# Performance work log

Hardware: AMD Instinct MI355X
Metric: run time of the kernel (lower is better)

Reference implementation:

```python
import jax, jax.numpy as jnp
import numpy as np

N_NODES = 10000
N_EDGES = 160000
F_IN, D, N_CLS = 300, 1024, 10
NEG_SLOPE = 0.2


def setup_inputs() -> dict:
    key = jax.random.key(0)
    ks = jax.random.split(key, 12)
    s = 0.05  # small init scale for numerical sanity
    return {
        "x": jax.random.normal(ks[0], (N_NODES, F_IN), jnp.float32),
        "edge_index": jax.random.randint(ks[1], (2, N_EDGES), 0, N_NODES, jnp.int64),
        "W1": jax.random.normal(ks[2], (F_IN, D), jnp.float32) * s,
        "att_src1": jax.random.normal(ks[3], (D,), jnp.float32) * s,
        "att_dst1": jax.random.normal(ks[4], (D,), jnp.float32) * s,
        "b1": jnp.zeros((D,), jnp.float32),
        "W2": jax.random.normal(ks[5], (D, D), jnp.float32) * s,
        "att_src2": jax.random.normal(ks[6], (D,), jnp.float32) * s,
        "att_dst2": jax.random.normal(ks[7], (D,), jnp.float32) * s,
        "b2": jnp.zeros((D,), jnp.float32),
        "fc_w": jax.random.normal(ks[8], (D, N_CLS), jnp.float32) * s,
        "fc_b": jnp.zeros((N_CLS,), jnp.float32),
    }


def gat_conv(x, src, dst, W, a_src, a_dst, b):
    # PyG GATConv, heads=1: h = x W; e_ij = leaky_relu(a_src.h_j + a_dst.h_i)
    h = x @ W                      # [N, D]
    e = jax.nn.leaky_relu((h @ a_src)[src] + (h @ a_dst)[dst], NEG_SLOPE)  # [E]
    # scatter-softmax over edges grouped by destination node
    m = jax.lax.stop_gradient(jax.ops.segment_max(e, dst, num_segments=N_NODES))
    ex = jnp.exp(e - m[dst])
    denom = jax.ops.segment_sum(ex, dst, num_segments=N_NODES)
    alpha = ex / denom[dst]        # [E]
    out = jax.ops.segment_sum(alpha[:, None] * h[src], dst, num_segments=N_NODES)
    return out + b


def reference(x, edge_index, W1, att_src1, att_dst1, b1,
              W2, att_src2, att_dst2, b2, fc_w, fc_b):
    loops = jnp.arange(N_NODES, dtype=edge_index.dtype)
    src = jnp.concatenate([edge_index[0], loops])  # add_self_loops=True
    dst = jnp.concatenate([edge_index[1], loops])
    emb = jax.nn.relu(gat_conv(x, src, dst, W1, att_src1, att_dst1, b1))
    emb = jax.nn.relu(gat_conv(emb, src, dst, W2, att_src2, att_dst2, b2))
    return jax.nn.softmax(emb @ fc_w + fc_b, axis=-1)
```

## Files before the change

### kernel.cpp

```cpp
#include <hip/hip_runtime.h>
#include <hip/hip_bf16.h>
#include <hip/hip_fp16.h>
#include <math.h>

#define N_NODES 10000
#define N_EDGES 160000
#define E_TOT   (N_EDGES + N_NODES)
#define F_IN    300
#define D       1024
#define N_CLS   10
#define NEG_SLOPE 0.2f

#define MP      10112
#define KP1     320
#define KP2     1024
#define WCAP    1024

typedef __attribute__((ext_vector_type(8))) _Float16 f16x8;
typedef __attribute__((ext_vector_type(4))) float f32x4;

#define GLOAD_LDS16(g, l) __builtin_amdgcn_global_load_lds( \
    (const __attribute__((address_space(1))) void*)(g), \
    (__attribute__((address_space(3))) void*)(l), 16, 0, 0)


__global__ void count_edges(const int* __restrict__ dst, int* __restrict__ deg) {
    int e = blockIdx.x * blockDim.x + threadIdx.x;
    if (e < N_EDGES) atomicAdd(&deg[dst[e]], 1);
}

__global__ void scan_offs(const int* __restrict__ deg, int* __restrict__ offs,
                          int* __restrict__ pos) {
    __shared__ int sbuf[1024];
    __shared__ int scarry;
    int t = threadIdx.x;
    if (t == 0) { scarry = 0; offs[0] = 0; }
    __syncthreads();
    for (int base = 0; base < N_NODES; base += 1024) {
        int v = (base + t < N_NODES) ? deg[base + t] : 0;
        sbuf[t] = v;
        __syncthreads();
        for (int off = 1; off < 1024; off <<= 1) {
            int add = (t >= off) ? sbuf[t - off] : 0;
            __syncthreads();
            sbuf[t] += add;
            __syncthreads();
        }
        int carry = scarry;
        if (base + t < N_NODES) {
            int incl = carry + sbuf[t];
            offs[base + t + 1] = incl;
            pos[base + t]      = incl - v;
        }
        __syncthreads();
        if (t == 1023) scarry = carry + sbuf[1023];
        __syncthreads();
    }
}

__global__ void scatter_edges(const int* __restrict__ src, const int* __restrict__ dst,
                              int* __restrict__ pos, int* __restrict__ ssrc) {
    int e = blockIdx.x * blockDim.x + threadIdx.x;
    if (e < N_EDGES) {
        int d = dst[e];
        int p = atomicAdd(&pos[d], 1);
        ssrc[p] = src[e];
    } else if (e < E_TOT) {
        int i = e - N_EDGES;
        int p = atomicAdd(&pos[i], 1);
        ssrc[p] = i;
    }
}


#define ZR1 (112 * KP1)
#define ZR2 (N_NODES * 20)
#define ZR3 (112 * KP2)
#define ZTOT (2*ZR1 + 2*ZR2 + 2*ZR3 + 2*N_NODES)

#define ZONE_A 331
#define ZONE_B 320
#define ZONE_C 1024
#define ZONE_D ((ZTOT + N_NODES + 255) / 256)

__global__ __launch_bounds__(256) void mega_prep(
        const float* __restrict__ W1, const float* __restrict__ as1,
        const float* __restrict__ ad1, const float* __restrict__ W2,
        const float* __restrict__ as2, const float* __restrict__ ad2,
        float* __restrict__ u1, float* __restrict__ v1,
        float* __restrict__ u2, float* __restrict__ v2,
        _Float16* __restrict__ BT1h, _Float16* __restrict__ BT2h,
        float* __restrict__ hs2, float* __restrict__ hd2,
        unsigned short* __restrict__ Ah1, unsigned short* __restrict__ Al1,
        unsigned short* __restrict__ Ah2, unsigned short* __restrict__ Al2,
        int* __restrict__ deg) {
    __shared__ float tile[32][33];
    int b = blockIdx.x;
    int t = threadIdx.x;

    if (b < ZONE_A) {
        int wid  = (b * 256 + t) >> 6;
        int lane = t & 63;
        const float* row; const float* a; const float* bb; float *du, *dv; int k;
        if (wid < F_IN) {
            k = wid; row = W1 + (size_t)k * D; a = as1; bb = ad1; du = u1; dv = v1;
        } else {
            k = wid - F_IN; row = W2 + (size_t)k * D; a = as2; bb = ad2; du = u2; dv = v2;
        }
        float s1 = 0.f, s2 = 0.f;
        for (int n = lane; n < D; n += 64) {
            float w = row[n];
            s1 += w * a[n];
            s2 += w * bb[n];
        }
        #pragma unroll
        for (int o = 32; o; o >>= 1) { s1 += __shfl_xor(s1, o); s2 += __shfl_xor(s2, o); }
        if (lane == 0) { du[k] = s1; dv[k] = s2; }
        return;
    }
    if (b < ZONE_A + ZONE_B + ZONE_C) {
        if (b < ZONE_A + ZONE_B) {
            int b2 = b - ZONE_A;
            int kb = b2 % (KP1 / 32), nb = b2 / (KP1 / 32);
            int k0 = kb * 32, n0 = nb * 32;
            int tx = t & 31, ty = t >> 5;
            #pragma unroll
            for (int j = 0; j < 32; j += 8) {
                int k = k0 + ty + j;
                tile[ty + j][tx] = (k < F_IN) ? W1[(size_t)k * D + n0 + tx] : 0.f;
            }
            __syncthreads();
            #pragma unroll
            for (int j = 0; j < 32; j += 8)
                BT1h[(size_t)(n0 + ty + j) * KP1 + k0 + tx] = (_Float16)tile[tx][ty + j];
        } else {
            int b2 = b - ZONE_A - ZONE_B;
            int kb = b2 & 31, nb = b2 >> 5;
            int k0 = kb * 32, n0 = nb * 32;
            int tx = t & 31, ty = t >> 5;
            #pragma unroll
            for (int j = 0; j < 32; j += 8) {
                int k = k0 + ty + j;
                tile[ty + j][tx] = W2[(size_t)k * D + n0 + tx];
            }
            __syncthreads();
            #pragma unroll
            for (int j = 0; j < 32; j += 8)
                BT2h[(size_t)(n0 + ty + j) * KP2 + k0 + tx] = (_Float16)tile[tx][ty + j];
        }
        return;
    }
    int idx = (b - ZONE_A - ZONE_B - ZONE_C) * 256 + t;
    if (idx >= ZTOT + N_NODES) return;
    if (idx >= ZTOT) { deg[idx - ZTOT] = 1; return; }
    if (idx < 2 * ZR1) {
        unsigned short* B = (idx < ZR1) ? Ah1 : Al1;
        int off = (idx < ZR1) ? idx : idx - ZR1;
        B[(size_t)N_NODES * KP1 + off] = 0;
    } else if ((idx -= 2 * ZR1) < 2 * ZR2) {
        unsigned short* B = (idx < ZR2) ? Ah1 : Al1;
        int off = (idx < ZR2) ? idx : idx - ZR2;
        int r = off / 20, c = 300 + off % 20;
        B[(size_t)r * KP1 + c] = 0;
    } else if ((idx -= 2 * ZR2) < 2 * ZR3) {
        unsigned short* B = (idx < ZR3) ? Ah2 : Al2;
        int off = (idx < ZR3) ? idx : idx - ZR3;
        B[(size_t)N_NODES * KP2 + off] = 0;
    } else {
        idx -= 2 * ZR3;
        if (idx < N_NODES) hs2[idx] = 0.f;
        else hd2[idx - N_NODES] = 0.f;
    }
}


__global__ void node_scores_x(const float* __restrict__ x, const float* __restrict__ u1,
                              const float* __restrict__ v1, float* __restrict__ hs,
                              float* __restrict__ hd) {
    int wid  = (int)((blockIdx.x * blockDim.x + threadIdx.x) >> 6);
    int lane = threadIdx.x & 63;
    if (wid >= N_NODES) return;
    const float* row = x + (size_t)wid * F_IN;
    float s1 = 0.f, s2 = 0.f;
    for (int k = lane; k < F_IN; k += 64) {
        float v = row[k];
        s1 += v * u1[k];
        s2 += v * v1[k];
    }
    #pragma unroll
    for (int o = 32; o; o >>= 1) { s1 += __shfl_xor(s1, o); s2 += __shfl_xor(s2, o); }
    if (lane == 0) { hs[wid] = s1; hd[wid] = s2; }
}


__global__ __launch_bounds__(256) void aggregate_x(
        const float* __restrict__ x, const float* __restrict__ hs,
        const float* __restrict__ hd, const int* __restrict__ offs,
        const int* __restrict__ ssrc, _Float16* __restrict__ outh,
        _Float16* __restrict__ outl) {
    int i = blockIdx.x;
    int t = threadIdx.x;
    int lane = t & 63;
    int wv = t >> 6;
    int start = offs[i], end = offs[i + 1];
    __shared__ float red[8];
    __shared__ float part[2][75][5];
    __shared__ float wcache[WCAP];
    float hdi = hd[i];

    float lmax = -INFINITY;
    for (int p = start + t; p < end; p += 256) {
        float s = hs[ssrc[p]] + hdi;
        s = (s >= 0.f) ? s : s * NEG_SLOPE;
        lmax = fmaxf(lmax, s);
    }
    #pragma unroll
    for (int o = 32; o; o >>= 1) lmax = fmaxf(lmax, __shfl_xor(lmax, o));
    if (lane == 0) red[wv] = lmax;
    __syncthreads();
    float m = fmaxf(fmaxf(red[0], red[1]), fmaxf(red[2], red[3]));

    float lsum = 0.f;
    for (int p = start + t; p < end; p += 256) {
        float s = hs[ssrc[p]] + hdi;
        s = (s >= 0.f) ? s : s * NEG_SLOPE;
        float ex = __expf(s - m);
        int q = p - start;
        if (q < WCAP) wcache[q] = ex;
        lsum += ex;
    }
    #pragma unroll
    for (int o = 32; o; o >>= 1) lsum += __shfl_xor(lsum, o);
    if (lane == 0) red[4 + wv] = lsum;
    __syncthreads();
    float inv = 1.0f / (red[4] + red[5] + red[6] + red[7]);
    bool cached = (end - start) <= WCAP;

    int g = t / 75;
    int s = t - g * 75;
    int c = s * 4;
    float4 a = {0.f, 0.f, 0.f, 0.f};
    if (t < 225) {
        int p = start + g;
        for (; p + 3 < end; p += 6) {
            int j0 = ssrc[p], j1 = ssrc[p + 3];
            float w0, w1;
            if (cached) { w0 = wcache[p - start]; w1 = wcache[p + 3 - start]; }
            else {
                float s0 = hs[j0] + hdi; s0 = (s0 >= 0.f) ? s0 : s0 * NEG_SLOPE;
                float s1 = hs[j1] + hdi; s1 = (s1 >= 0.f) ? s1 : s1 * NEG_SLOPE;
                w0 = __expf(s0 - m); w1 = __expf(s1 - m);
            }
            float4 v0 = *(const float4*)(x + (size_t)j0 * F_IN + c);
            float4 v1 = *(const float4*)(x + (size_t)j1 * F_IN + c);
            a.x += w0 * v0.x + w1 * v1.x;
            a.y += w0 * v0.y + w1 * v1.y;
            a.z += w0 * v0.z + w1 * v1.z;
            a.w += w0 * v0.w + w1 * v1.w;
        }
        if (p < end) {
            int j0 = ssrc[p];
            float w0;
            if (cached) w0 = wcache[p - start];
            else {
                float s0 = hs[j0] + hdi; s0 = (s0 >= 0.f) ? s0 : s0 * NEG_SLOPE;
                w0 = __expf(s0 - m);
            }
            float4 v0 = *(const float4*)(x + (size_t)j0 * F_IN + c);
            a.x += w0 * v0.x; a.y += w0 * v0.y; a.z += w0 * v0.z; a.w += w0 * v0.w;
        }
    }
    if (t < 225 && g > 0) {
        part[g - 1][s][0] = a.x; part[g - 1][s][1] = a.y;
        part[g - 1][s][2] = a.z; part[g - 1][s][3] = a.w;
    }
    __syncthreads();
    if (t < 75) {
        a.x += part[0][t][0] + part[1][t][0];
        a.y += part[0][t][1] + part[1][t][1];
        a.z += part[0][t][2] + part[1][t][2];
        a.w += part[0][t][3] + part[1][t][3];
        float rv[4] = {a.x * inv, a.y * inv, a.z * inv, a.w * inv};
        _Float16 hi4[4], lo4[4];
        #pragma unroll
        for (int q = 0; q < 4; ++q) {
            _Float16 hi = (_Float16)rv[q];
            hi4[q] = hi;
            lo4[q] = (_Float16)(rv[q] - (float)hi);
        }
        *(float2*)(outh + (size_t)i * KP1 + c) = *(float2*)hi4;
        *(float2*)(outl + (size_t)i * KP1 + c) = *(float2*)lo4;
    }
}


__global__ __launch_bounds__(256) void aggregate_d(
        const _Float16* __restrict__ h, const float* __restrict__ hs,
        const float* __restrict__ hd, const int* __restrict__ offs,
        const int* __restrict__ ssrc, _Float16* __restrict__ outh,
        _Float16* __restrict__ outl) {
    int i = blockIdx.x;
    int t = threadIdx.x;
    int lane = t & 63;
    int wv = t >> 6;
    int start = offs[i], end = offs[i + 1];
    __shared__ float red[8];
    __shared__ float part[128][9];
    __shared__ float wcache[WCAP];
    float hdi = hd[i];

    float lmax = -INFINITY;
    for (int p = start + t; p < end; p += 256) {
        float s = hs[ssrc[p]] + hdi;
        s = (s >= 0.f) ? s : s * NEG_SLOPE;
        lmax = fmaxf(lmax, s);
    }
    #pragma unroll
    for (int o = 32; o; o >>= 1) lmax = fmaxf(lmax, __shfl_xor(lmax, o));
    if (lane == 0) red[wv] = lmax;
    __syncthreads();
    float m = fmaxf(fmaxf(red[0], red[1]), fmaxf(red[2], red[3]));

    float lsum = 0.f;
    for (int p = start + t; p < end; p += 256) {
        float s = hs[ssrc[p]] + hdi;
        s = (s >= 0.f) ? s : s * NEG_SLOPE;
        float ex = __expf(s - m);
        int q = p - start;
        if (q < WCAP) wcache[q] = ex;
        lsum += ex;
    }
    #pragma unroll
    for (int o = 32; o; o >>= 1) lsum += __shfl_xor(lsum, o);
    if (lane == 0) red[4 + wv] = lsum;
    __syncthreads();
    float inv = 1.0f / (red[4] + red[5] + red[6] + red[7]);
    bool cached = (end - start) <= WCAP;

    int g = t >> 7;
    int s = t & 127;
    int c = s * 8;
    float a0[8] = {}, a1[8] = {}, a2[8] = {}, a3[8] = {};
    int p = start + g;
    for (; p + 6 < end; p += 8) {
        int j0 = ssrc[p], j1 = ssrc[p + 2], j2 = ssrc[p + 4], j3 = ssrc[p + 6];
        float w0, w1, w2, w3;
        if (cached) {
            int q = p - start;
            w0 = wcache[q]; w1 = wcache[q + 2]; w2 = wcache[q + 4]; w3 = wcache[q + 6];
        } else {
            float s0 = hs[j0] + hdi; s0 = (s0 >= 0.f) ? s0 : s0 * NEG_SLOPE;
            float s1 = hs[j1] + hdi; s1 = (s1 >= 0.f) ? s1 : s1 * NEG_SLOPE;
            float s2 = hs[j2] + hdi; s2 = (s2 >= 0.f) ? s2 : s2 * NEG_SLOPE;
            float s3 = hs[j3] + hdi; s3 = (s3 >= 0.f) ? s3 : s3 * NEG_SLOPE;
            w0 = __expf(s0 - m); w1 = __expf(s1 - m);
            w2 = __expf(s2 - m); w3 = __expf(s3 - m);
        }
        f16x8 v0 = *(const f16x8*)(h + (size_t)j0 * D + c);
        f16x8 v1 = *(const f16x8*)(h + (size_t)j1 * D + c);
        f16x8 v2 = *(const f16x8*)(h + (size_t)j2 * D + c);
        f16x8 v3 = *(const f16x8*)(h + (size_t)j3 * D + c);
        #pragma unroll
        for (int q = 0; q < 8; ++q) {
            a0[q] += w0 * (float)v0[q];
            a1[q] += w1 * (float)v1[q];
            a2[q] += w2 * (float)v2[q];
            a3[q] += w3 * (float)v3[q];
        }
    }
    for (; p < end; p += 2) {
        int j0 = ssrc[p];
        float w0;
        if (cached) w0 = wcache[p - start];
        else {
            float s0 = hs[j0] + hdi; s0 = (s0 >= 0.f) ? s0 : s0 * NEG_SLOPE;
            w0 = __expf(s0 - m);
        }
        f16x8 v0 = *(const f16x8*)(h + (size_t)j0 * D + c);
        #pragma unroll
        for (int q = 0; q < 8; ++q) a0[q] += w0 * (float)v0[q];
    }
    float af[8];
    #pragma unroll
    for (int q = 0; q < 8; ++q) af[q] = (a0[q] + a1[q]) + (a2[q] + a3[q]);
    if (g == 1) {
        #pragma unroll
        for (int q = 0; q < 8; ++q) part[s][q] = af[q];
    }
    __syncthreads();
    if (t < 128) {
        _Float16 hi8[8], lo8[8];
        #pragma unroll
        for (int q = 0; q < 8; ++q) {
            float rv = (af[q] + part[t][q]) * inv;
            _Float16 hi = (_Float16)rv;
            hi8[q] = hi;
            lo8[q] = (_Float16)(rv - (float)hi);
        }
        *(float4*)(outh + (size_t)i * KP2 + c) = *(float4*)hi8;
        *(float4*)(outl + (size_t)i * KP2 + c) = *(float4*)lo8;
    }
}


__global__ __launch_bounds__(256) void gemm_split_mfma(
        const _Float16* __restrict__ Ah, const _Float16* __restrict__ Al,
        const _Float16* __restrict__ BTh,
        float* __restrict__ Cf, _Float16* __restrict__ Ch,
        const float* __restrict__ bias,
        const float* __restrict__ asrc, const float* __restrict__ adst,
        float* __restrict__ hs, float* __restrict__ hd,
        int Mreal, int Kp, int dots) {
    __shared__ char lds[3 * 24576];
    const int t    = threadIdx.x;
    const int lane = t & 63;
    const int wid  = t >> 6;
    const int chunkg = (int)gridDim.x >> 3;
    const int vid  = ((int)blockIdx.x & 7) * chunkg + ((int)blockIdx.x >> 3);
    const int n0 = (vid & 7) * 128;
    const int m0 = (vid >> 3) * 128;
    const int wr = (wid >> 1) * 64;
    const int wc = (wid & 1) * 64;
    const int fr = lane & 15;
    const int kg = lane >> 4;

    const int r0 = t >> 2, s0 = t & 3;
    const int r1 = r0 + 64;
    const int g0 = (s0 ^ ((r0 >> 1) & 3)) << 3;
    const int g1 = (s0 ^ ((r1 >> 1) & 3)) << 3;
    const size_t oA0 = (size_t)(m0 + r0) * Kp + g0;
    const size_t oA1 = (size_t)(m0 + r1) * Kp + g1;
    const size_t oB0 = (size_t)(n0 + r0) * Kp + g0;
    const size_t oB1 = (size_t)(n0 + r1) * Kp + g1;
    const int ko = (kg ^ ((fr >> 1) & 3)) << 4;

    f32x4 acc[4][4] = {};
    const int nsteps = Kp >> 5;

    auto STAGE = [&](int b, int kb) {
        char* base = lds + b * 24576;
        GLOAD_LDS16(Ah  + oA0 + kb, base + t * 16);
        GLOAD_LDS16(Ah  + oA1 + kb, base + 4096  + t * 16);
        GLOAD_LDS16(Al  + oA0 + kb, base + 8192  + t * 16);
        GLOAD_LDS16(Al  + oA1 + kb, base + 12288 + t * 16);
        GLOAD_LDS16(BTh + oB0 + kb, base + 16384 + t * 16);
        GLOAD_LDS16(BTh + oB1 + kb, base + 20480 + t * 16);
    };

    STAGE(0, 0);
    STAGE(1, 32);

    for (int k = 0; k < nsteps; ++k) {
        if (k + 2 < nsteps) STAGE((k + 2) % 3, (k + 2) << 5);
        int rem = nsteps - 1 - k;
        if (rem >= 2)      asm volatile("s_waitcnt vmcnt(12)" ::: "memory");
        else if (rem == 1) asm volatile("s_waitcnt vmcnt(6)" ::: "memory");
        else               asm volatile("s_waitcnt vmcnt(0)" ::: "memory");
        __builtin_amdgcn_s_barrier();
        __builtin_amdgcn_sched_barrier(0);
        char* base = lds + (k % 3) * 24576;
        f16x8 ah[4], al[4], bh[4];
        #pragma unroll
        for (int f = 0; f < 4; ++f) {
            int ra = (wr + f * 16 + fr) * 64 + ko;
            int rb = (wc + f * 16 + fr) * 64 + ko;
            ah[f] = *(const f16x8*)(base + ra);
            al[f] = *(const f16x8*)(base + 8192 + ra);
            bh[f] = *(const f16x8*)(base + 16384 + rb);
        }
        #pragma unroll
        for (int fm = 0; fm < 4; ++fm)
            #pragma unroll
            for (int fn = 0; fn < 4; ++fn)
                acc[fm][fn] = __builtin_amdgcn_mfma_f32_16x16x32_f16(
                    ah[fm], bh[fn], acc[fm][fn], 0, 0, 0);
        #pragma unroll
        for (int fm = 0; fm < 4; ++fm)
            #pragma unroll
            for (int fn = 0; fn < 4; ++fn)
                acc[fm][fn] = __builtin_amdgcn_mfma_f32_16x16x32_f16(
                    al[fm], bh[fn], acc[fm][fn], 0, 0, 0);
        __builtin_amdgcn_s_barrier();
    }

    float bv[4];
    #pragma unroll
    for (int fn = 0; fn < 4; ++fn) bv[fn] = bias[n0 + wc + fn * 16 + fr];
    #pragma unroll
    for (int fm = 0; fm < 4; ++fm) {
        int mb = m0 + wr + fm * 16 + kg * 4;
        #pragma unroll
        for (int fn = 0; fn < 4; ++fn) {
            int cn = n0 + wc + fn * 16 + fr;
            #pragma unroll
            for (int j = 0; j < 4; ++j) {
                float r = fmaxf(acc[fm][fn][j] + bv[fn], 0.f);
                acc[fm][fn][j] = r;
                int m = mb + j;
                if (m < Mreal) {
                    if (Cf) Cf[(size_t)m * 1024 + cn] = r;
                    else    Ch[(size_t)m * 1024 + cn] = (_Float16)r;
                }
            }
        }
    }

    if (dots) {
        float av[4], dv[4];
        #pragma unroll
        for (int fn = 0; fn < 4; ++fn) {
            int cn = n0 + wc + fn * 16 + fr;
            av[fn] = asrc[cn];
            dv[fn] = adst[cn];
        }
        #pragma unroll
        for (int fm = 0; fm < 4; ++fm) {
            #pragma unroll
            for (int j = 0; j < 4; ++j) {
                float v1 = acc[fm][0][j] * av[0] + acc[fm][1][j] * av[1]
                         + acc[fm][2][j] * av[2] + acc[fm][3][j] * av[3];
                float v2 = acc[fm][0][j] * dv[0] + acc[fm][1][j] * dv[1]
                         + acc[fm][2][j] * dv[2] + acc[fm][3][j] * dv[3];
                #pragma unroll
                for (int o = 1; o < 16; o <<= 1) {
                    v1 += __shfl_xor(v1, o);
                    v2 += __shfl_xor(v2, o);
                }
                int m = m0 + wr + fm * 16 + kg * 4 + j;
                if (fr == 0 && m < Mreal) {
                    atomicAdd(&hs[m], v1);
                    atomicAdd(&hd[m], v2);
                }
            }
        }
    }
}


__global__ void fc_softmax(const _Float16* __restrict__ emb, const float* __restrict__ fcw,
                           const float* __restrict__ fcb, float* __restrict__ out) {
    int wid  = (int)((blockIdx.x * blockDim.x + threadIdx.x) >> 6);
    int lane = threadIdx.x & 63;
    if (wid >= N_NODES) return;
    float acc[N_CLS] = {};
    const _Float16* row = emb + (size_t)wid * D;
    for (int k = lane * 8; k < D; k += 512) {
        f16x8 v = *(const f16x8*)(row + k);
        #pragma unroll
        for (int q = 0; q < 8; ++q) {
            float vv = (float)v[q];
            #pragma unroll
            for (int c = 0; c < N_CLS; ++c) acc[c] += vv * fcw[(k + q) * N_CLS + c];
        }
    }
    #pragma unroll
    for (int c = 0; c < N_CLS; ++c) {
        #pragma unroll
        for (int o = 32; o; o >>= 1) acc[c] += __shfl_xor(acc[c], o);
    }
    if (lane == 0) {
        float logit[N_CLS];
        float m = -INFINITY;
        #pragma unroll
        for (int c = 0; c < N_CLS; ++c) { logit[c] = acc[c] + fcb[c]; m = fmaxf(m, logit[c]); }
        float s = 0.f;
        #pragma unroll
        for (int c = 0; c < N_CLS; ++c) { logit[c] = __expf(logit[c] - m); s += logit[c]; }
        float invs = 1.0f / s;
        #pragma unroll
        for (int c = 0; c < N_CLS; ++c) out[(size_t)wid * N_CLS + c] = logit[c] * invs;
    }
}


extern "C" void kernel_launch(void* const* d_in, const int* in_sizes, int n_in,
                              void* d_out, int out_size, void* d_ws, size_t ws_size,
                              hipStream_t stream) {
    const float* x        = (const float*)d_in[0];
    const int*   ei       = (const int*)d_in[1];
    const float* W1       = (const float*)d_in[2];
    const float* att_src1 = (const float*)d_in[3];
    const float* att_dst1 = (const float*)d_in[4];
    const float* b1       = (const float*)d_in[5];
    const float* W2       = (const float*)d_in[6];
    const float* att_src2 = (const float*)d_in[7];
    const float* att_dst2 = (const float*)d_in[8];
    const float* b2       = (const float*)d_in[9];
    const float* fc_w     = (const float*)d_in[10];
    const float* fc_b     = (const float*)d_in[11];
    float* out = (float*)d_out;

    const int* src = ei;
    const int* dst = ei + N_EDGES;

    char* w = (char*)d_ws;
    #define ALLOC(name, bytes) char* name = w; w += (((size_t)(bytes) + 255) & ~(size_t)255)
    ALLOC(p_emb1h, (size_t)N_NODES * D * 2);
    ALLOC(p_emb2h, (size_t)N_NODES * D * 2);
    ALLOC(p_hs1,   (size_t)N_NODES * 4);
    ALLOC(p_hd1,   (size_t)N_NODES * 4);
    ALLOC(p_hs2,   (size_t)N_NODES * 4);
    ALLOC(p_hd2,   (size_t)N_NODES * 4);
    ALLOC(p_deg,   (size_t)N_NODES * 4);
    ALLOC(p_offs,  (size_t)(N_NODES + 1) * 4);
    ALLOC(p_pos,   (size_t)N_NODES * 4);
    ALLOC(p_ssrc,  (size_t)E_TOT * 4);
    ALLOC(p_u1,    (size_t)F_IN * 4);
    ALLOC(p_v1,    (size_t)F_IN * 4);
    ALLOC(p_u2,    (size_t)D * 4);
    ALLOC(p_v2,    (size_t)D * 4);
    ALLOC(p_as1,   (size_t)2 * MP * KP1 * 2);
    ALLOC(p_as2,   (size_t)2 * MP * KP2 * 2);
    ALLOC(p_bt1,   (size_t)D * KP1 * 2);
    ALLOC(p_bt2,   (size_t)D * KP2 * 2);
    #undef ALLOC

    _Float16* emb1h = (_Float16*)p_emb1h;
    _Float16* emb2h = (_Float16*)p_emb2h;
    float* hs1  = (float*)p_hs1;
    float* hd1  = (float*)p_hd1;
    float* hs2  = (float*)p_hs2;
    float* hd2  = (float*)p_hd2;
    int*   deg  = (int*)p_deg;
    int*   offs = (int*)p_offs;
    int*   pos  = (int*)p_pos;
    int*   ssrc = (int*)p_ssrc;
    float* u1 = (float*)p_u1; float* v1 = (float*)p_v1;
    float* u2 = (float*)p_u2; float* v2 = (float*)p_v2;
    _Float16* Ah1  = (_Float16*)p_as1;
    _Float16* Al1  = Ah1 + (size_t)MP * KP1;
    _Float16* Ah2  = (_Float16*)p_as2;
    _Float16* Al2  = Ah2 + (size_t)MP * KP2;
    _Float16* BT1h = (_Float16*)p_bt1;
    _Float16* BT2h = (_Float16*)p_bt2;

    mega_prep<<<ZONE_A + ZONE_B + ZONE_C + ZONE_D, 256, 0, stream>>>(
        W1, att_src1, att_dst1, W2, att_src2, att_dst2,
        u1, v1, u2, v2, BT1h, BT2h, hs2, hd2,
        (unsigned short*)Ah1, (unsigned short*)Al1,
        (unsigned short*)Ah2, (unsigned short*)Al2, deg);

    count_edges<<<(N_EDGES + 255) / 256, 256, 0, stream>>>(dst, deg);
    scan_offs<<<1, 1024, 0, stream>>>(deg, offs, pos);
    scatter_edges<<<(E_TOT + 255) / 256, 256, 0, stream>>>(src, dst, pos, ssrc);

    const int gemmGrid = (D / 128) * (MP / 128);

    node_scores_x<<<(N_NODES * 64 + 255) / 256, 256, 0, stream>>>(x, u1, v1, hs1, hd1);
    aggregate_x<<<N_NODES, 256, 0, stream>>>(x, hs1, hd1, offs, ssrc, Ah1, Al1);
    gemm_split_mfma<<<gemmGrid, 256, 0, stream>>>(Ah1, Al1, BT1h,
                                                  (float*)nullptr, emb1h, b1,
                                                  u2, v2, hs2, hd2, N_NODES, KP1, 1);

    aggregate_d<<<N_NODES, 256, 0, stream>>>(emb1h, hs2, hd2, offs, ssrc, Ah2, Al2);
    gemm_split_mfma<<<gemmGrid, 256, 0, stream>>>(Ah2, Al2, BT2h,
                                                  (float*)nullptr, emb2h, b2,
                                                  (const float*)nullptr, (const float*)nullptr,
                                                  (float*)nullptr, (float*)nullptr,
                                                  N_NODES, KP2, 0);

    fc_softmax<<<(N_NODES * 64 + 255) / 256, 256, 0, stream>>>(emb2h, fc_w, fc_b, out);
}
```

Measured before the change: 342.2 us.

## Fuse final FC projection into layer-2 GEMM epilogue and use double-buffered staging

The second GEMM no longer writes the fp16 layer-2 embedding. Each block instead projects its relu'd tile onto fc_w, reduces across lanes with shuffles and atomically adds partial logits into a zeroed buffer. A small softmax kernel then finishes the output. This removes a 20 MB write and read-back, but adds many float atomics (8 column blocks per logit) and extra epilogue register pressure. Separately, the GEMM pipeline drops from triple to double LDS buffering, which cuts LDS use but reduces load-latency hiding.

```diff
diff --git a/kernel.cpp b/kernel.cpp
--- a/kernel.cpp
+++ b/kernel.cpp
@@ -76,7 +76,8 @@
 #define ZR1 (112 * KP1)
 #define ZR2 (N_NODES * 20)
 #define ZR3 (112 * KP2)
-#define ZTOT (2*ZR1 + 2*ZR2 + 2*ZR3 + 2*N_NODES)
+#define ZR4 (N_NODES * N_CLS)
+#define ZTOT (2*ZR1 + 2*ZR2 + 2*ZR3 + 2*N_NODES + ZR4)
 
 #define ZONE_A 331
 #define ZONE_B 320
@@ -93,7 +94,7 @@
         float* __restrict__ hs2, float* __restrict__ hd2,
         unsigned short* __restrict__ Ah1, unsigned short* __restrict__ Al1,
         unsigned short* __restrict__ Ah2, unsigned short* __restrict__ Al2,
-        int* __restrict__ deg) {
+        int* __restrict__ deg, float* __restrict__ logits) {
     __shared__ float tile[32][33];
     int b = blockIdx.x;
     int t = threadIdx.x;
@@ -169,7 +170,8 @@
     } else {
         idx -= 2 * ZR3;
         if (idx < N_NODES) hs2[idx] = 0.f;
-        else hd2[idx - N_NODES] = 0.f;
+        else if (idx < 2 * N_NODES) hd2[idx - N_NODES] = 0.f;
+        else logits[idx - 2 * N_NODES] = 0.f;
     }
 }
 
@@ -406,12 +408,12 @@
 __global__ __launch_bounds__(256) void gemm_split_mfma(
         const _Float16* __restrict__ Ah, const _Float16* __restrict__ Al,
         const _Float16* __restrict__ BTh,
-        float* __restrict__ Cf, _Float16* __restrict__ Ch,
-        const float* __restrict__ bias,
+        _Float16* __restrict__ Ch, const float* __restrict__ bias,
         const float* __restrict__ asrc, const float* __restrict__ adst,
         float* __restrict__ hs, float* __restrict__ hd,
+        const float* __restrict__ fcw, float* __restrict__ logits,
         int Mreal, int Kp, int dots) {
-    __shared__ char lds[3 * 24576];
+    __shared__ char lds[2 * 24576];
     const int t    = threadIdx.x;
     const int lane = t & 63;
     const int wid  = t >> 6;
@@ -448,17 +450,17 @@
     };
 
     STAGE(0, 0);
-    STAGE(1, 32);
 
     for (int k = 0; k < nsteps; ++k) {
-        if (k + 2 < nsteps) STAGE((k + 2) % 3, (k + 2) << 5);
-        int rem = nsteps - 1 - k;
-        if (rem >= 2)      asm volatile("s_waitcnt vmcnt(12)" ::: "memory");
-        else if (rem == 1) asm volatile("s_waitcnt vmcnt(6)" ::: "memory");
-        else               asm volatile("s_waitcnt vmcnt(0)" ::: "memory");
+        if (k + 1 < nsteps) {
+            STAGE((k + 1) & 1, (k + 1) << 5);
+            asm volatile("s_waitcnt vmcnt(6)" ::: "memory");
+        } else {
+            asm volatile("s_waitcnt vmcnt(0)" ::: "memory");
+        }
         __builtin_amdgcn_s_barrier();
         __builtin_amdgcn_sched_barrier(0);
-        char* base = lds + (k % 3) * 24576;
+        char* base = lds + (k & 1) * 24576;
         f16x8 ah[4], al[4], bh[4];
         #pragma unroll
         for (int f = 0; f < 4; ++f) {
@@ -497,10 +499,7 @@
                 float r = fmaxf(acc[fm][fn][j] + bv[fn], 0.f);
                 acc[fm][fn][j] = r;
                 int m = mb + j;
-                if (m < Mreal) {
-                    if (Cf) Cf[(size_t)m * 1024 + cn] = r;
-                    else    Ch[(size_t)m * 1024 + cn] = (_Float16)r;
-                }
+                if (Ch && m < Mreal) Ch[(size_t)m * 1024 + cn] = (_Float16)r;
             }
         }
     }
@@ -534,42 +533,54 @@
             }
         }
     }
-}
-
-
-__global__ void fc_softmax(const _Float16* __restrict__ emb, const float* __restrict__ fcw,
-                           const float* __restrict__ fcb, float* __restrict__ out) {
-    int wid  = (int)((blockIdx.x * blockDim.x + threadIdx.x) >> 6);
-    int lane = threadIdx.x & 63;
-    if (wid >= N_NODES) return;
-    float acc[N_CLS] = {};
-    const _Float16* row = emb + (size_t)wid * D;
-    for (int k = lane * 8; k < D; k += 512) {
-        f16x8 v = *(const f16x8*)(row + k);
-        #pragma unroll
-        for (int q = 0; q < 8; ++q) {
-            float vv = (float)v[q];
-            #pragma unroll
-            for (int c = 0; c < N_CLS; ++c) acc[c] += vv * fcw[(k + q) * N_CLS + c];
-        }
-    }
-    #pragma unroll
-    for (int c = 0; c < N_CLS; ++c) {
-        #pragma unroll
-        for (int o = 32; o; o >>= 1) acc[c] += __shfl_xor(acc[c], o);
-    }
-    if (lane == 0) {
-        float logit[N_CLS];
-        float m = -INFINITY;
-        #pragma unroll
-        for (int c = 0; c < N_CLS; ++c) { logit[c] = acc[c] + fcb[c]; m = fmaxf(m, logit[c]); }
-        float s = 0.f;
-        #pragma unroll
-        for (int c = 0; c < N_CLS; ++c) { logit[c] = __expf(logit[c] - m); s += logit[c]; }
-        float invs = 1.0f / s;
-        #pragma unroll
-        for (int c = 0; c < N_CLS; ++c) out[(size_t)wid * N_CLS + c] = logit[c] * invs;
-    }
+
+    if (fcw) {
+        float fw[4][N_CLS];
+        #pragma unroll
+        for (int fn = 0; fn < 4; ++fn) {
+            int cn = n0 + wc + fn * 16 + fr;
+            #pragma unroll
+            for (int c = 0; c < N_CLS; ++c) fw[fn][c] = fcw[cn * N_CLS + c];
+        }
+        #pragma unroll
+        for (int fm = 0; fm < 4; ++fm) {
+            #pragma unroll
+            for (int j = 0; j < 4; ++j) {
+                float lg[N_CLS];
+                #pragma unroll
+                for (int c = 0; c < N_CLS; ++c)
+                    lg[c] = acc[fm][0][j] * fw[0][c] + acc[fm][1][j] * fw[1][c]
+                          + acc[fm][2][j] * fw[2][c] + acc[fm][3][j] * fw[3][c];
+                #pragma unroll
+                for (int c = 0; c < N_CLS; ++c) {
+                    #pragma unroll
+                    for (int o = 1; o < 16; o <<= 1) lg[c] += __shfl_xor(lg[c], o);
+                }
+                int m = m0 + wr + fm * 16 + kg * 4 + j;
+                if (fr == 0 && m < Mreal) {
+                    #pragma unroll
+                    for (int c = 0; c < N_CLS; ++c) atomicAdd(&logits[m * N_CLS + c], lg[c]);
+                }
+            }
+        }
+    }
+}
+
+
+__global__ void logits_softmax(const float* __restrict__ logits,
+                               const float* __restrict__ fcb, float* __restrict__ out) {
+    int i = blockIdx.x * blockDim.x + threadIdx.x;
+    if (i >= N_NODES) return;
+    float lg[N_CLS];
+    float m = -INFINITY;
+    #pragma unroll
+    for (int c = 0; c < N_CLS; ++c) { lg[c] = logits[i * N_CLS + c] + fcb[c]; m = fmaxf(m, lg[c]); }
+    float s = 0.f;
+    #pragma unroll
+    for (int c = 0; c < N_CLS; ++c) { lg[c] = __expf(lg[c] - m); s += lg[c]; }
+    float invs = 1.0f / s;
+    #pragma unroll
+    for (int c = 0; c < N_CLS; ++c) out[i * N_CLS + c] = lg[c] * invs;
 }
 
 
@@ -595,8 +606,8 @@
 
     char* w = (char*)d_ws;
     #define ALLOC(name, bytes) char* name = w; w += (((size_t)(bytes) + 255) & ~(size_t)255)
-    ALLOC(p_emb1h, (size_t)N_NODES * D * 2);
-    ALLOC(p_emb2h, (size_t)N_NODES * D * 2);
+    ALLOC(p_emb1h,  (size_t)N_NODES * D * 2);
+    ALLOC(p_logits, (size_t)N_NODES * N_CLS * 4);
     ALLOC(p_hs1,   (size_t)N_NODES * 4);
     ALLOC(p_hd1,   (size_t)N_NODES * 4);
     ALLOC(p_hs2,   (size_t)N_NODES * 4);
@@ -616,7 +627,7 @@
     #undef ALLOC
 
     _Float16* emb1h = (_Float16*)p_emb1h;
-    _Float16* emb2h = (_Float16*)p_emb2h;
+    float* logits = (float*)p_logits;
     float* hs1  = (float*)p_hs1;
     float* hd1  = (float*)p_hd1;
     float* hs2  = (float*)p_hs2;
@@ -638,7 +649,7 @@
         W1, att_src1, att_dst1, W2, att_src2, att_dst2,
         u1, v1, u2, v2, BT1h, BT2h, hs2, hd2,
         (unsigned short*)Ah1, (unsigned short*)Al1,
-        (unsigned short*)Ah2, (unsigned short*)Al2, deg);
+        (unsigned short*)Ah2, (unsigned short*)Al2, deg, logits);
 
     count_edges<<<(N_EDGES + 255) / 256, 256, 0, stream>>>(dst, deg);
     scan_offs<<<1, 1024, 0, stream>>>(deg, offs, pos);
@@ -648,16 +659,17 @@
 
     node_scores_x<<<(N_NODES * 64 + 255) / 256, 256, 0, stream>>>(x, u1, v1, hs1, hd1);
     aggregate_x<<<N_NODES, 256, 0, stream>>>(x, hs1, hd1, offs, ssrc, Ah1, Al1);
-    gemm_split_mfma<<<gemmGrid, 256, 0, stream>>>(Ah1, Al1, BT1h,
-                                                  (float*)nullptr, emb1h, b1,
-                                                  u2, v2, hs2, hd2, N_NODES, KP1, 1);
+    gemm_split_mfma<<<gemmGrid, 256, 0, stream>>>(Ah1, Al1, BT1h, emb1h, b1,
+                                                  u2, v2, hs2, hd2,
+                                                  (const float*)nullptr, (float*)nullptr,
+                                                  N_NODES, KP1, 1);
 
     aggregate_d<<<N_NODES, 256, 0, stream>>>(emb1h, hs2, hd2, offs, ssrc, Ah2, Al2);
     gemm_split_mfma<<<gemmGrid, 256, 0, stream>>>(Ah2, Al2, BT2h,
-                                                  (float*)nullptr, emb2h, b2,
+                                                  (_Float16*)nullptr, b2,
                                                   (const float*)nullptr, (const float*)nullptr,
                                                   (float*)nullptr, (float*)nullptr,
-                                                  N_NODES, KP2, 0);
-
-    fc_softmax<<<(N_NODES * 64 + 255) / 256, 256, 0, stream>>>(emb2h, fc_w, fc_b, out);
-}
+                                                  fc_w, logits, N_NODES, KP2, 0);
+
+    logits_softmax<<<(N_NODES + 255) / 256, 256, 0, stream>>>(logits, fc_b, out);
+}
```

Result: slower. 458.6 us (+34.0%).
